# Performance work log

Hardware: AMD Instinct MI355X
Metric: run time of the kernel (lower is better)

Reference implementation:

```python
import jax, jax.numpy as jnp
import numpy as np

N_NODES = 50000
NEG_SLOPE = 0.2


def gat_conv(x, src, dst, W, a_src, a_dst, bias, heads):
    # x: [N, Fin]; W: [Fin, heads*C]; a_src/a_dst: [heads, C]; bias: [heads*C]
    n = x.shape[0]
    h = (x @ W).reshape(n, heads, -1)              # [N, H, C]
    alpha_src = jnp.einsum('nhc,hc->nh', h, a_src)  # [N, H]
    alpha_dst = jnp.einsum('nhc,hc->nh', h, a_dst)  # [N, H]
    e = alpha_src[src] + alpha_dst[dst]             # [E, H]
    e = jax.nn.leaky_relu(e, NEG_SLOPE)
    # segment softmax over edges grouped by destination node
    m = jax.ops.segment_max(e, dst, num_segments=n)          # [N, H]
    e = jnp.exp(e - jax.lax.stop_gradient(m)[dst])
    s = jax.ops.segment_sum(e, dst, num_segments=n)          # [N, H]
    alpha = e / (s[dst] + 1e-16)                              # [E, H]
    msg = h[src] * alpha[:, :, None]                          # [E, H, C]
    out = jax.ops.segment_sum(msg, dst, num_segments=n)      # [N, H, C]
    return out.reshape(n, -1) + bias


def add_self_loops(edge_index, n):
    loops = jnp.arange(n, dtype=edge_index.dtype)
    src = jnp.concatenate([edge_index[0], loops])
    dst = jnp.concatenate([edge_index[1], loops])
    return src, dst


def setup_inputs() -> dict:
    key = jax.random.key(0)
    ks = jax.random.split(key, 10)
    num_features, num_classes, heads1, c1 = 128, 40, 8, 32
    n_edges = 800000
    x = jax.random.normal(ks[0], (N_NODES, num_features), dtype=jnp.float32)
    edge_index = jax.random.randint(ks[1], (2, n_edges), 0, N_NODES, dtype=jnp.int64)
    sc = 0.1
    W1 = jax.random.normal(ks[2], (num_features, heads1 * c1), dtype=jnp.float32) * sc
    a_src1 = jax.random.normal(ks[3], (heads1, c1), dtype=jnp.float32) * sc
    a_dst1 = jax.random.normal(ks[4], (heads1, c1), dtype=jnp.float32) * sc
    b1 = jnp.zeros((heads1 * c1,), dtype=jnp.float32)
    W2 = jax.random.normal(ks[5], (heads1 * c1, num_classes), dtype=jnp.float32) * sc
    a_src2 = jax.random.normal(ks[6], (1, num_classes), dtype=jnp.float32) * sc
    a_dst2 = jax.random.normal(ks[7], (1, num_classes), dtype=jnp.float32) * sc
    b2 = jnp.zeros((num_classes,), dtype=jnp.float32)
    return {"x": x, "edge_index": edge_index, "W1": W1, "a_src1": a_src1,
            "a_dst1": a_dst1, "b1": b1, "W2": W2, "a_src2": a_src2,
            "a_dst2": a_dst2, "b2": b2}


def reference(x, edge_index, W1, a_src1, a_dst1, b1, W2, a_src2, a_dst2, b2):
    src, dst = add_self_loops(edge_index, x.shape[0])
    h = gat_conv(x, src, dst, W1, a_src1, a_dst1, b1, heads=8)
    h = jax.nn.elu(h)
    h = gat_conv(h, src, dst, W2, a_src2, a_dst2, b2, heads=1)
    return jax.nn.log_softmax(h, axis=1)
```

## Files before the change

kernel.cpp:

```cpp
#include <hip/hip_runtime.h>
#include <math.h>

#define NNODES 50000
#define F_IN   128
#define F1     256
#define H1N    8
#define NCLS   40
#define NEG    0.2f
#define MNEG  -3.0e38f
#define SCAN_BLOCKS 196
#define ACAP   256

typedef unsigned int uint32;
typedef __attribute__((ext_vector_type(8))) short short8v;
typedef __attribute__((ext_vector_type(4))) float f32x4;

__device__ __forceinline__ float leaky(float x) { return x > 0.f ? x : NEG * x; }

__device__ __forceinline__ unsigned short f2bf(float f) {
  uint32 u = __float_as_uint(f);
  u = (u + 0x7FFFu + ((u >> 16) & 1u)) >> 16;
  return (unsigned short)u;
}
__device__ __forceinline__ float bf_lo(uint32 u) { return __uint_as_float(u << 16); }
__device__ __forceinline__ float bf_hi(uint32 u) { return __uint_as_float(u & 0xFFFF0000u); }

__global__ __launch_bounds__(256) void convx_k(const float* __restrict__ x,
                                               unsigned short* __restrict__ xb) {
  int i = blockIdx.x * 256 + threadIdx.x;
  float4 v = ((const float4*)x)[i];
  uint2 o;
  o.x = (uint32)f2bf(v.x) | ((uint32)f2bf(v.y) << 16);
  o.y = (uint32)f2bf(v.z) | ((uint32)f2bf(v.w) << 16);
  ((uint2*)xb)[i] = o;
}

__global__ __launch_bounds__(256) void convw_k(const float* __restrict__ W,
                                               unsigned short* __restrict__ Wt) {
  int id = blockIdx.x * 256 + threadIdx.x;
  int k = id >> 8, c = id & 255;
  Wt[c * 128 + k] = f2bf(W[id]);
}

__global__ __launch_bounds__(256) void convw2_k(const float* __restrict__ W2,
                                                unsigned short* __restrict__ Wt2) {
  int id = blockIdx.x * 256 + threadIdx.x;
  int c = id >> 8, k = id & 255;
  Wt2[c * 256 + k] = (c < NCLS) ? f2bf(W2[k * NCLS + c]) : (unsigned short)0;
}

__global__ __launch_bounds__(256) void gemm1_mfma_k(
    const unsigned short* __restrict__ xb, const unsigned short* __restrict__ Wt,
    const float* __restrict__ asrc, const float* __restrict__ adst,
    unsigned short* __restrict__ h1b, float* __restrict__ as1,
    float* __restrict__ ad1) {
  const int lane = threadIdx.x & 63;
  const int wv   = threadIdx.x >> 6;
  const int row0 = blockIdx.x * 64 + wv * 16;
  if (row0 >= NNODES) return;
  const int lrow = lane & 15;
  const int kgrp = lane >> 4;

  const short8v* xp = (const short8v*)xb;
  short8v a[4];
  #pragma unroll
  for (int ks = 0; ks < 4; ++ks)
    a[ks] = xp[(row0 + lrow) * 16 + ks * 4 + kgrp];

  const short8v* wp = (const short8v*)Wt;
  float ps[4] = {0.f, 0.f, 0.f, 0.f};
  float pd[4] = {0.f, 0.f, 0.f, 0.f};

  for (int n = 0; n < 16; ++n) {
    f32x4 acc = {0.f, 0.f, 0.f, 0.f};
    #pragma unroll
    for (int ks = 0; ks < 4; ++ks) {
      short8v b = wp[(n * 16 + lrow) * 16 + ks * 4 + kgrp];
      acc = __builtin_amdgcn_mfma_f32_16x16x32_bf16(a[ks], b, acc, 0, 0, 0);
    }
    const int col = n * 16 + lrow;
    const float ascv = asrc[col];
    const float advv = adst[col];
    #pragma unroll
    for (int r = 0; r < 4; ++r) {
      int row = row0 + kgrp * 4 + r;
      h1b[(long)row * F1 + col] = f2bf(acc[r]);
      ps[r] = fmaf(acc[r], ascv, ps[r]);
      pd[r] = fmaf(acc[r], advv, pd[r]);
    }
    if (n & 1) {
      const int head = n >> 1;
      #pragma unroll
      for (int r = 0; r < 4; ++r) {
        #pragma unroll
        for (int mask = 1; mask <= 8; mask <<= 1) {
          ps[r] += __shfl_xor(ps[r], mask, 64);
          pd[r] += __shfl_xor(pd[r], mask, 64);
        }
      }
      if (lrow == 0) {
        #pragma unroll
        for (int r = 0; r < 4; ++r) {
          int row = row0 + kgrp * 4 + r;
          as1[row * H1N + head] = ps[r];
          ad1[row * H1N + head] = pd[r];
        }
      }
      #pragma unroll
      for (int r = 0; r < 4; ++r) { ps[r] = 0.f; pd[r] = 0.f; }
    }
  }
}

__global__ __launch_bounds__(256) void hist_k(const int* __restrict__ ei,
                                              int* __restrict__ deg, int E, int ET) {
  int e = blockIdx.x * 256 + threadIdx.x;
  if (e >= ET) return;
  int d = (e < E) ? ei[E + e] : e - E;
  atomicAdd(&deg[d], 1);
}

__global__ __launch_bounds__(256) void partsum_k(const int* __restrict__ deg,
                                                 int* __restrict__ blocksum) {
  int idx = blockIdx.x * 256 + threadIdx.x;
  int v = (idx < NNODES) ? deg[idx] : 0;
  #pragma unroll
  for (int m = 32; m >= 1; m >>= 1) v += __shfl_xor(v, m, 64);
  __shared__ int sh[4];
  if ((threadIdx.x & 63) == 0) sh[threadIdx.x >> 6] = v;
  __syncthreads();
  if (threadIdx.x == 0) blocksum[blockIdx.x] = sh[0] + sh[1] + sh[2] + sh[3];
}

__global__ __launch_bounds__(256) void scanblocks_k(const int* __restrict__ blocksum,
                                                    int* __restrict__ blockoff) {
  __shared__ int sh[256];
  int t = threadIdx.x;
  int v = (t < SCAN_BLOCKS) ? blocksum[t] : 0;
  sh[t] = v;
  __syncthreads();
  for (int off = 1; off < 256; off <<= 1) {
    int u = (t >= off) ? sh[t - off] : 0;
    __syncthreads();
    sh[t] += u;
    __syncthreads();
  }
  if (t < SCAN_BLOCKS) blockoff[t] = (t == 0) ? 0 : sh[t - 1];
}

__global__ __launch_bounds__(256) void rowstart_k(const int* __restrict__ deg,
                                                  const int* __restrict__ blockoff,
                                                  int* __restrict__ row_start,
                                                  int* __restrict__ cursor, int ET) {
  __shared__ int sh[256];
  int t = threadIdx.x;
  int idx = blockIdx.x * 256 + t;
  int v = (idx < NNODES) ? deg[idx] : 0;
  sh[t] = v;
  __syncthreads();
  for (int off = 1; off < 256; off <<= 1) {
    int u = (t >= off) ? sh[t - off] : 0;
    __syncthreads();
    sh[t] += u;
    __syncthreads();
  }
  int incl = sh[t];
  int base = blockoff[blockIdx.x];
  if (idx < NNODES) {
    int rs = base + incl - v;
    row_start[idx] = rs;
    cursor[idx] = rs;
    if (idx == NNODES - 1) row_start[NNODES] = base + incl;
  }
}

__global__ __launch_bounds__(256) void scatter_k(const int* __restrict__ ei,
                                                 int* __restrict__ cursor,
                                                 int* __restrict__ csr_src, int E, int ET) {
  int e = blockIdx.x * 256 + threadIdx.x;
  if (e >= ET) return;
  int s, d;
  if (e < E) { s = ei[e]; d = ei[E + e]; } else { s = d = e - E; }
  int pos = atomicAdd(&cursor[d], 1);
  csr_src[pos] = s;
}

__global__ __launch_bounds__(128) void agg1_k(
    const int* __restrict__ row_start, const int* __restrict__ csr_src,
    const float* __restrict__ as1, const float* __restrict__ ad1,
    const uint32* __restrict__ h1b, const float* __restrict__ b1,
    uint32* __restrict__ x2b) {
  __shared__ float alpha_lds[ACAP][H1N];
  __shared__ float partial[128];
  __shared__ float rs_lds[8];
  const int d = blockIdx.x;
  const int t = threadIdx.x;
  const int r0 = row_start[d], r1e = row_start[d + 1];

  {
    const int hh = t & 7, slot = t >> 3;
    const float adv = ad1[d * 8 + hh];
    float sum = 0.f;
    for (int i = r0 + slot; i < r1e; i += 16) {
      float ex = __expf(leaky(as1[csr_src[i] * 8 + hh] + adv));
      sum += ex;
      int idx = i - r0;
      if (idx < ACAP) alpha_lds[idx][hh] = ex;
    }
    partial[t] = sum;
  }
  __syncthreads();
  if (t < 8) {
    float s = 0.f;
    #pragma unroll
    for (int j = 0; j < 16; ++j) s += partial[t + 8 * j];
    rs_lds[t] = 1.f / (s + 1e-16f);
  }
  __syncthreads();

  const int h = t >> 4;
  const float adh = ad1[d * 8 + h];
  float acc0 = 0.f, acc1 = 0.f;
  int i = r0;
  for (; i + 2 <= r1e; i += 2) {
    int s0 = csr_src[i], s1 = csr_src[i + 1];
    int i0 = i - r0, i1 = i0 + 1;
    float a0 = (i0 < ACAP) ? alpha_lds[i0][h]
                           : __expf(leaky(as1[s0 * 8 + h] + adh));
    float a1 = (i1 < ACAP) ? alpha_lds[i1][h]
                           : __expf(leaky(as1[s1 * 8 + h] + adh));
    uint32 v0 = h1b[s0 * 128 + t];
    uint32 v1 = h1b[s1 * 128 + t];
    acc0 = fmaf(bf_lo(v0), a0, acc0);
    acc1 = fmaf(bf_hi(v0), a0, acc1);
    acc0 = fmaf(bf_lo(v1), a1, acc0);
    acc1 = fmaf(bf_hi(v1), a1, acc1);
  }
  if (i < r1e) {
    int s0 = csr_src[i];
    int i0 = i - r0;
    float a0 = (i0 < ACAP) ? alpha_lds[i0][h]
                           : __expf(leaky(as1[s0 * 8 + h] + adh));
    uint32 v0 = h1b[s0 * 128 + t];
    acc0 = fmaf(bf_lo(v0), a0, acc0);
    acc1 = fmaf(bf_hi(v0), a0, acc1);
  }
  float rch = rs_lds[h];
  acc0 *= rch;
  acc1 *= rch;
  float2 b = ((const float2*)b1)[t];
  float o0 = acc0 + b.x, o1 = acc1 + b.y;
  o0 = o0 > 0.f ? o0 : expm1f(o0);
  o1 = o1 > 0.f ? o1 : expm1f(o1);
  x2b[(long)d * 128 + t] = (uint32)f2bf(o0) | ((uint32)f2bf(o1) << 16);
}

__global__ __launch_bounds__(256) void gemm2_mfma_k(
    const unsigned short* __restrict__ x2b, const unsigned short* __restrict__ Wt2,
    const float* __restrict__ a_src2, const float* __restrict__ a_dst2,
    float* __restrict__ h2, float* __restrict__ as2, float* __restrict__ ad2) {
  const int lane = threadIdx.x & 63;
  const int wv   = threadIdx.x >> 6;
  const int row0 = blockIdx.x * 64 + wv * 16;
  if (row0 >= NNODES) return;
  const int lrow = lane & 15;
  const int kgrp = lane >> 4;

  const short8v* xp = (const short8v*)x2b;
  short8v a[8];
  #pragma unroll
  for (int ks = 0; ks < 8; ++ks)
    a[ks] = xp[(row0 + lrow) * 32 + ks * 4 + kgrp];

  const short8v* wp = (const short8v*)Wt2;
  float ps[4] = {0.f, 0.f, 0.f, 0.f};
  float pd[4] = {0.f, 0.f, 0.f, 0.f};

  #pragma unroll
  for (int n = 0; n < 3; ++n) {
    f32x4 acc = {0.f, 0.f, 0.f, 0.f};
    #pragma unroll
    for (int ks = 0; ks < 8; ++ks) {
      short8v b = wp[(n * 16 + lrow) * 32 + ks * 4 + kgrp];
      acc = __builtin_amdgcn_mfma_f32_16x16x32_bf16(a[ks], b, acc, 0, 0, 0);
    }
    const int col = n * 16 + lrow;
    const bool valid = col < NCLS;
    const float asv = valid ? a_src2[col] : 0.f;
    const float adv = valid ? a_dst2[col] : 0.f;
    #pragma unroll
    for (int r = 0; r < 4; ++r) {
      int row = row0 + kgrp * 4 + r;
      if (valid) h2[(long)row * NCLS + col] = acc[r];
      ps[r] = fmaf(acc[r], asv, ps[r]);
      pd[r] = fmaf(acc[r], adv, pd[r]);
    }
  }
  #pragma unroll
  for (int r = 0; r < 4; ++r) {
    #pragma unroll
    for (int mask = 1; mask <= 8; mask <<= 1) {
      ps[r] += __shfl_xor(ps[r], mask, 64);
      pd[r] += __shfl_xor(pd[r], mask, 64);
    }
  }
  if (lrow == 0) {
    #pragma unroll
    for (int r = 0; r < 4; ++r) {
      int row = row0 + kgrp * 4 + r;
      as2[row] = ps[r];
      ad2[row] = pd[r];
    }
  }
}

__global__ __launch_bounds__(256) void agg2_k(
    const int* __restrict__ row_start, const int* __restrict__ csr_src,
    const float* __restrict__ as2, const float* __restrict__ ad2,
    const float* __restrict__ h2, const float* __restrict__ b2,
    float* __restrict__ out) {
  int wave = threadIdx.x >> 6, lane = threadIdx.x & 63;
  int d = blockIdx.x * 4 + wave;
  if (d >= NNODES) return;
  int r0 = row_start[d], r1e = row_start[d + 1];
  const float add = ad2[d];

  float sum = 0.f;
  for (int i = r0 + lane; i < r1e; i += 64)
    sum += __expf(leaky(as2[csr_src[i]] + add));
  #pragma unroll
  for (int mask = 1; mask <= 32; mask <<= 1) sum += __shfl_xor(sum, mask, 64);
  float rcp = 1.f / (sum + 1e-16f);

  float acc = 0.f;
  int i = r0;
  for (; i + 2 <= r1e; i += 2) {
    int s0 = csr_src[i], s1 = csr_src[i + 1];
    float a0 = __expf(leaky(as2[s0] + add));
    float a1 = __expf(leaky(as2[s1] + add));
    float v0 = (lane < NCLS) ? h2[(long)s0 * NCLS + lane] : 0.f;
    float v1 = (lane < NCLS) ? h2[(long)s1 * NCLS + lane] : 0.f;
    acc = fmaf(v0, a0, acc);
    acc = fmaf(v1, a1, acc);
  }
  if (i < r1e) {
    int s0 = csr_src[i];
    float a0 = __expf(leaky(as2[s0] + add));
    float v0 = (lane < NCLS) ? h2[(long)s0 * NCLS + lane] : 0.f;
    acc = fmaf(v0, a0, acc);
  }
  acc *= rcp;

  float v = (lane < NCLS) ? acc + b2[lane] : MNEG;
  float mm = v;
  #pragma unroll
  for (int mask = 1; mask <= 32; mask <<= 1) mm = fmaxf(mm, __shfl_xor(mm, mask, 64));
  float ex = (lane < NCLS) ? __expf(v - mm) : 0.f;
  float se = ex;
  #pragma unroll
  for (int mask = 1; mask <= 32; mask <<= 1) se += __shfl_xor(se, mask, 64);
  if (lane < NCLS) out[(long)d * NCLS + lane] = v - mm - __logf(se);
}

extern "C" void kernel_launch(void* const* d_in, const int* in_sizes, int n_in,
                              void* d_out, int out_size, void* d_ws, size_t ws_size,
                              hipStream_t stream) {
  const float* x      = (const float*)d_in[0];
  const int*   ei     = (const int*)d_in[1];
  const float* W1     = (const float*)d_in[2];
  const float* a_src1 = (const float*)d_in[3];
  const float* a_dst1 = (const float*)d_in[4];
  const float* b1     = (const float*)d_in[5];
  const float* W2     = (const float*)d_in[6];
  const float* a_src2 = (const float*)d_in[7];
  const float* a_dst2 = (const float*)d_in[8];
  const float* b2     = (const float*)d_in[9];
  float* out = (float*)d_out;

  const int E  = in_sizes[1] / 2;
  const int ET = E + NNODES;

  float* ws = (float*)d_ws;
  unsigned short* h1b = (unsigned short*)ws;
  float* h2     = ws;
  float* as2    = ws + 2000000;
  float* ad2    = ws + 2050000;
  uint32* x2b   = (uint32*)(ws + 6400000);
  unsigned short* xb = (unsigned short*)(ws + 9700000);
  unsigned short* Wt = (unsigned short*)(ws + 13000000);
  unsigned short* Wt2 = (unsigned short*)(ws + 13100000);
  float* as1    = ws + 19200000;
  float* ad1    = ws + 19600000;
  int* row_start = (int*)(ws + 26800000);
  int* cursor    = row_start + 50001;
  int* deg       = cursor + 50000;
  int* csr_src   = deg + 50000;
  int* blocksum  = csr_src + 850000;
  int* blockoff  = blocksum + 256;

  hipMemsetAsync(deg, 0, NNODES * sizeof(int), stream);

  hist_k<<<(ET + 255) / 256, 256, 0, stream>>>(ei, deg, E, ET);
  partsum_k<<<SCAN_BLOCKS, 256, 0, stream>>>(deg, blocksum);
  scanblocks_k<<<1, 256, 0, stream>>>(blocksum, blockoff);
  rowstart_k<<<SCAN_BLOCKS, 256, 0, stream>>>(deg, blockoff, row_start, cursor, ET);
  scatter_k<<<(ET + 255) / 256, 256, 0, stream>>>(ei, cursor, csr_src, E, ET);

  convx_k<<<6250, 256, 0, stream>>>(x, xb);
  convw_k<<<128, 256, 0, stream>>>(W1, Wt);
  convw2_k<<<48, 256, 0, stream>>>(W2, Wt2);
  gemm1_mfma_k<<<(NNODES + 63) / 64, 256, 0, stream>>>(xb, Wt, a_src1, a_dst1,
                                                       h1b, as1, ad1);
  agg1_k<<<NNODES, 128, 0, stream>>>(row_start, csr_src, as1, ad1,
                                     (const uint32*)h1b, b1, x2b);

  gemm2_mfma_k<<<(NNODES + 63) / 64, 256, 0, stream>>>(
      (const unsigned short*)x2b, Wt2, a_src2, a_dst2, h2, as2, ad2);
  agg2_k<<<NNODES / 4, 256, 0, stream>>>(row_start, csr_src, as2, ad2, h2, b2, out);
}
```

Before: 394.4 us.

## Use single-wave agg1 blocks, store layer-2 features as bf16, cache agg2 alphas

agg1 moves from 128 to 64 threads per destination node. Each lane now handles 4 channels with uint2 loads, and the block-wide partial-sum reduction becomes wave shuffles, which drops one barrier. gemm2 writes h2 as bf16 instead of fp32, halving the gathered bytes per edge in agg2. agg2 caches the first 64 edge exponentials in LDS so it does not recompute exp and re-gather as2. This adds bf16 rounding error in layer 2 and a block barrier in agg2.

```diff
diff --git a/kernel.cpp b/kernel.cpp
--- a/kernel.cpp
+++ b/kernel.cpp
@@ -9,7 +9,7 @@
 #define NEG    0.2f
 #define MNEG  -3.0e38f
 #define SCAN_BLOCKS 196
-#define ACAP   256
+#define ACAP   64
 
 typedef unsigned int uint32;
 typedef __attribute__((ext_vector_type(8))) short short8v;
@@ -24,6 +24,9 @@
 }
 __device__ __forceinline__ float bf_lo(uint32 u) { return __uint_as_float(u << 16); }
 __device__ __forceinline__ float bf_hi(uint32 u) { return __uint_as_float(u & 0xFFFF0000u); }
+__device__ __forceinline__ float bfu(unsigned short u) {
+  return __uint_as_float((uint32)u << 16);
+}
 
 __global__ __launch_bounds__(256) void convx_k(const float* __restrict__ x,
                                                unsigned short* __restrict__ xb) {
@@ -185,13 +188,12 @@
   csr_src[pos] = s;
 }
 
-__global__ __launch_bounds__(128) void agg1_k(
+__global__ __launch_bounds__(64) void agg1_k(
     const int* __restrict__ row_start, const int* __restrict__ csr_src,
     const float* __restrict__ as1, const float* __restrict__ ad1,
     const uint32* __restrict__ h1b, const float* __restrict__ b1,
     uint32* __restrict__ x2b) {
   __shared__ float alpha_lds[ACAP][H1N];
-  __shared__ float partial[128];
   __shared__ float rs_lds[8];
   const int d = blockIdx.x;
   const int t = threadIdx.x;
@@ -201,64 +203,71 @@
     const int hh = t & 7, slot = t >> 3;
     const float adv = ad1[d * 8 + hh];
     float sum = 0.f;
-    for (int i = r0 + slot; i < r1e; i += 16) {
+    for (int i = r0 + slot; i < r1e; i += 8) {
       float ex = __expf(leaky(as1[csr_src[i] * 8 + hh] + adv));
       sum += ex;
       int idx = i - r0;
       if (idx < ACAP) alpha_lds[idx][hh] = ex;
     }
-    partial[t] = sum;
+    sum += __shfl_xor(sum, 8, 64);
+    sum += __shfl_xor(sum, 16, 64);
+    sum += __shfl_xor(sum, 32, 64);
+    if (t < 8) rs_lds[t] = 1.f / (sum + 1e-16f);
   }
   __syncthreads();
-  if (t < 8) {
-    float s = 0.f;
-    #pragma unroll
-    for (int j = 0; j < 16; ++j) s += partial[t + 8 * j];
-    rs_lds[t] = 1.f / (s + 1e-16f);
-  }
-  __syncthreads();
-
-  const int h = t >> 4;
+
+  const int h = t >> 3;
   const float adh = ad1[d * 8 + h];
-  float acc0 = 0.f, acc1 = 0.f;
+  float a0 = 0.f, a1 = 0.f, a2 = 0.f, a3 = 0.f;
   int i = r0;
   for (; i + 2 <= r1e; i += 2) {
     int s0 = csr_src[i], s1 = csr_src[i + 1];
-    int i0 = i - r0, i1 = i0 + 1;
-    float a0 = (i0 < ACAP) ? alpha_lds[i0][h]
+    int i0 = i - r0;
+    float w0 = (i0 < ACAP) ? alpha_lds[i0][h]
                            : __expf(leaky(as1[s0 * 8 + h] + adh));
-    float a1 = (i1 < ACAP) ? alpha_lds[i1][h]
-                           : __expf(leaky(as1[s1 * 8 + h] + adh));
-    uint32 v0 = h1b[s0 * 128 + t];
-    uint32 v1 = h1b[s1 * 128 + t];
-    acc0 = fmaf(bf_lo(v0), a0, acc0);
-    acc1 = fmaf(bf_hi(v0), a0, acc1);
-    acc0 = fmaf(bf_lo(v1), a1, acc0);
-    acc1 = fmaf(bf_hi(v1), a1, acc1);
+    float w1 = (i0 + 1 < ACAP) ? alpha_lds[i0 + 1][h]
+                               : __expf(leaky(as1[s1 * 8 + h] + adh));
+    uint2 v0 = ((const uint2*)(h1b + (long)s0 * 128))[t];
+    uint2 v1 = ((const uint2*)(h1b + (long)s1 * 128))[t];
+    a0 = fmaf(bf_lo(v0.x), w0, a0);
+    a1 = fmaf(bf_hi(v0.x), w0, a1);
+    a2 = fmaf(bf_lo(v0.y), w0, a2);
+    a3 = fmaf(bf_hi(v0.y), w0, a3);
+    a0 = fmaf(bf_lo(v1.x), w1, a0);
+    a1 = fmaf(bf_hi(v1.x), w1, a1);
+    a2 = fmaf(bf_lo(v1.y), w1, a2);
+    a3 = fmaf(bf_hi(v1.y), w1, a3);
   }
   if (i < r1e) {
     int s0 = csr_src[i];
     int i0 = i - r0;
-    float a0 = (i0 < ACAP) ? alpha_lds[i0][h]
+    float w0 = (i0 < ACAP) ? alpha_lds[i0][h]
                            : __expf(leaky(as1[s0 * 8 + h] + adh));
-    uint32 v0 = h1b[s0 * 128 + t];
-    acc0 = fmaf(bf_lo(v0), a0, acc0);
-    acc1 = fmaf(bf_hi(v0), a0, acc1);
-  }
-  float rch = rs_lds[h];
-  acc0 *= rch;
-  acc1 *= rch;
-  float2 b = ((const float2*)b1)[t];
-  float o0 = acc0 + b.x, o1 = acc1 + b.y;
+    uint2 v0 = ((const uint2*)(h1b + (long)s0 * 128))[t];
+    a0 = fmaf(bf_lo(v0.x), w0, a0);
+    a1 = fmaf(bf_hi(v0.x), w0, a1);
+    a2 = fmaf(bf_lo(v0.y), w0, a2);
+    a3 = fmaf(bf_hi(v0.y), w0, a3);
+  }
+  const float rch = rs_lds[h];
+  float4 b = ((const float4*)b1)[t];
+  float o0 = a0 * rch + b.x, o1 = a1 * rch + b.y;
+  float o2 = a2 * rch + b.z, o3 = a3 * rch + b.w;
   o0 = o0 > 0.f ? o0 : expm1f(o0);
   o1 = o1 > 0.f ? o1 : expm1f(o1);
-  x2b[(long)d * 128 + t] = (uint32)f2bf(o0) | ((uint32)f2bf(o1) << 16);
+  o2 = o2 > 0.f ? o2 : expm1f(o2);
+  o3 = o3 > 0.f ? o3 : expm1f(o3);
+  uint2 o;
+  o.x = (uint32)f2bf(o0) | ((uint32)f2bf(o1) << 16);
+  o.y = (uint32)f2bf(o2) | ((uint32)f2bf(o3) << 16);
+  ((uint2*)(x2b + (long)d * 128))[t] = o;
 }
 
 __global__ __launch_bounds__(256) void gemm2_mfma_k(
     const unsigned short* __restrict__ x2b, const unsigned short* __restrict__ Wt2,
     const float* __restrict__ a_src2, const float* __restrict__ a_dst2,
-    float* __restrict__ h2, float* __restrict__ as2, float* __restrict__ ad2) {
+    unsigned short* __restrict__ h2b, float* __restrict__ as2,
+    float* __restrict__ ad2) {
   const int lane = threadIdx.x & 63;
   const int wv   = threadIdx.x >> 6;
   const int row0 = blockIdx.x * 64 + wv * 16;
@@ -291,7 +300,7 @@
     #pragma unroll
     for (int r = 0; r < 4; ++r) {
       int row = row0 + kgrp * 4 + r;
-      if (valid) h2[(long)row * NCLS + col] = acc[r];
+      if (valid) h2b[(long)row * NCLS + col] = f2bf(acc[r]);
       ps[r] = fmaf(acc[r], asv, ps[r]);
       pd[r] = fmaf(acc[r], adv, pd[r]);
     }
@@ -317,36 +326,46 @@
 __global__ __launch_bounds__(256) void agg2_k(
     const int* __restrict__ row_start, const int* __restrict__ csr_src,
     const float* __restrict__ as2, const float* __restrict__ ad2,
-    const float* __restrict__ h2, const float* __restrict__ b2,
+    const unsigned short* __restrict__ h2b, const float* __restrict__ b2,
     float* __restrict__ out) {
+  __shared__ float acache[4][ACAP];
   int wave = threadIdx.x >> 6, lane = threadIdx.x & 63;
   int d = blockIdx.x * 4 + wave;
-  if (d >= NNODES) return;
   int r0 = row_start[d], r1e = row_start[d + 1];
   const float add = ad2[d];
 
   float sum = 0.f;
-  for (int i = r0 + lane; i < r1e; i += 64)
-    sum += __expf(leaky(as2[csr_src[i]] + add));
+  for (int i = r0 + lane; i < r1e; i += 64) {
+    float ex = __expf(leaky(as2[csr_src[i]] + add));
+    int idx = i - r0;
+    if (idx < ACAP) acache[wave][idx] = ex;
+    sum += ex;
+  }
   #pragma unroll
   for (int mask = 1; mask <= 32; mask <<= 1) sum += __shfl_xor(sum, mask, 64);
   float rcp = 1.f / (sum + 1e-16f);
+  __syncthreads();
 
   float acc = 0.f;
   int i = r0;
   for (; i + 2 <= r1e; i += 2) {
     int s0 = csr_src[i], s1 = csr_src[i + 1];
-    float a0 = __expf(leaky(as2[s0] + add));
-    float a1 = __expf(leaky(as2[s1] + add));
-    float v0 = (lane < NCLS) ? h2[(long)s0 * NCLS + lane] : 0.f;
-    float v1 = (lane < NCLS) ? h2[(long)s1 * NCLS + lane] : 0.f;
+    int i0 = i - r0;
+    float a0 = (i0 < ACAP) ? acache[wave][i0]
+                           : __expf(leaky(as2[s0] + add));
+    float a1 = (i0 + 1 < ACAP) ? acache[wave][i0 + 1]
+                               : __expf(leaky(as2[s1] + add));
+    float v0 = (lane < NCLS) ? bfu(h2b[(long)s0 * NCLS + lane]) : 0.f;
+    float v1 = (lane < NCLS) ? bfu(h2b[(long)s1 * NCLS + lane]) : 0.f;
     acc = fmaf(v0, a0, acc);
     acc = fmaf(v1, a1, acc);
   }
   if (i < r1e) {
     int s0 = csr_src[i];
-    float a0 = __expf(leaky(as2[s0] + add));
-    float v0 = (lane < NCLS) ? h2[(long)s0 * NCLS + lane] : 0.f;
+    int i0 = i - r0;
+    float a0 = (i0 < ACAP) ? acache[wave][i0]
+                           : __expf(leaky(as2[s0] + add));
+    float v0 = (lane < NCLS) ? bfu(h2b[(long)s0 * NCLS + lane]) : 0.f;
     acc = fmaf(v0, a0, acc);
   }
   acc *= rcp;
@@ -382,7 +401,7 @@
 
   float* ws = (float*)d_ws;
   unsigned short* h1b = (unsigned short*)ws;
-  float* h2     = ws;
+  unsigned short* h2b = (unsigned short*)ws;
   float* as2    = ws + 2000000;
   float* ad2    = ws + 2050000;
   uint32* x2b   = (uint32*)(ws + 6400000);
@@ -411,10 +430,10 @@
   convw2_k<<<48, 256, 0, stream>>>(W2, Wt2);
   gemm1_mfma_k<<<(NNODES + 63) / 64, 256, 0, stream>>>(xb, Wt, a_src1, a_dst1,
                                                        h1b, as1, ad1);
-  agg1_k<<<NNODES, 128, 0, stream>>>(row_start, csr_src, as1, ad1,
-                                     (const uint32*)h1b, b1, x2b);
+  agg1_k<<<NNODES, 64, 0, stream>>>(row_start, csr_src, as1, ad1,
+                                    (const uint32*)h1b, b1, x2b);
 
   gemm2_mfma_k<<<(NNODES + 63) / 64, 256, 0, stream>>>(
-      (const unsigned short*)x2b, Wt2, a_src2, a_dst2, h2, as2, ad2);
-  agg2_k<<<NNODES / 4, 256, 0, stream>>>(row_start, csr_src, as2, ad2, h2, b2, out);
-}
+      (const unsigned short*)x2b, Wt2, a_src2, a_dst2, h2b, as2, ad2);
+  agg2_k<<<NNODES / 4, 256, 0, stream>>>(row_start, csr_src, as2, ad2, h2b, b2, out);
+}
```

Measured after the change: 388.6 us. About the same (-1.5%).
